# Optimization experiments

Hardware: AMD Instinct MI355X
Metric: run time of the kernel (lower is better)

The kernel has to match this reference:

```python
import jax, jax.numpy as jnp
import numpy as np

B, S, D = 2, 2048, 2048
NH, NKV, HD = 16, 4, 128
EPS = 1e-6


def rmsnorm(x, w, eps=EPS):
    # torch.nn.RMSNorm: x * rsqrt(mean(x^2) + eps) * weight
    ms = jnp.mean(jnp.square(x), axis=-1, keepdims=True)
    return x * jax.lax.rsqrt(ms + eps) * w


def apply_rotary_emb(x, freqs_cis):
    # x: (B, S, H, HD); freqs_cis: (S, HD//2, 2) -> pairwise complex rotation (gpt-fast style)
    xs = x.reshape(*x.shape[:-1], -1, 2)          # (B,S,H,HD//2,2)
    fc = freqs_cis[None, :, None, :, :]           # (1,S,1,HD//2,2)
    xr, xi = xs[..., 0], xs[..., 1]
    fr, fi = fc[..., 0], fc[..., 1]
    out = jnp.stack([xr * fr - xi * fi, xi * fr + xr * fi], axis=-1)
    return out.reshape(x.shape)


def setup_inputs() -> dict:
    key = jax.random.key(0)
    ks = jax.random.split(key, 4)
    x = jax.random.normal(ks[0], (B, S, D), dtype=jnp.float32)
    freqs_cis = jax.random.normal(ks[1], (S, HD // 2, 2), dtype=jnp.float32)
    wqkv = jax.random.normal(ks[2], ((NH + 2 * NKV) * HD, D), dtype=jnp.float32) * (D ** -0.5)
    wo = jax.random.normal(ks[3], (NH * HD, D), dtype=jnp.float32).T * ((NH * HD) ** -0.5)
    wo = jnp.asarray(wo)  # (D, NH*HD) torch layout (out,in)
    q_norm_w = jnp.ones((HD,), dtype=jnp.float32)
    k_norm_w = jnp.ones((HD,), dtype=jnp.float32)
    return {"x": x, "freqs_cis": freqs_cis, "wqkv": wqkv, "wo": wo,
            "q_norm_w": q_norm_w, "k_norm_w": k_norm_w}


def reference(x, freqs_cis, wqkv, wo, q_norm_w, k_norm_w):
    b, s, _ = x.shape
    q_size, kv_size = NH * HD, NKV * HD
    qkv = jnp.einsum('bsd,ed->bse', x, wqkv)  # fused QKV projection
    q, k, v = jnp.split(qkv, [q_size, q_size + kv_size], axis=-1)
    q = q.reshape(b, s, NH, HD)
    k = k.reshape(b, s, NKV, HD)
    v = v.reshape(b, s, NKV, HD)
    q = rmsnorm(q, q_norm_w)
    k = rmsnorm(k, k_norm_w)
    q = apply_rotary_emb(q, freqs_cis)
    k = apply_rotary_emb(k, freqs_cis)
    # GQA: repeat_interleave KV heads to NH
    rep = NH // NKV
    k = jnp.repeat(k, rep, axis=2)  # (b,s,NH,HD)
    v = jnp.repeat(v, rep, axis=2)
    scale = 1.0 / np.sqrt(HD)
    scores = jnp.einsum('bqhd,bkhd->bhqk', q, k) * scale
    causal = jnp.tril(jnp.ones((s, s), dtype=bool))
    scores = jnp.where(causal[None, None], scores, -jnp.inf)
    attn = jax.nn.softmax(scores, axis=-1)
    y = jnp.einsum('bhqk,bkhd->bqhd', attn, v)
    y = y.reshape(b, s, q_size)
    return jnp.einsum('bse,de->bsd', y, wo)
```

## Files before the change

kernel.cpp:

```cpp
#include <hip/hip_runtime.h>
#include <math.h>

constexpr int B_ = 2, S_ = 2048, D_ = 2048, NH_ = 16, NKV_ = 4, HD_ = 128;
constexpr int EQKV_ = (NH_ + 2 * NKV_) * HD_;
constexpr int M_ = B_ * S_;
constexpr float EPS_ = 1e-6f;
constexpr float QSCALE_ = 0.08838834764831845f;

typedef __attribute__((ext_vector_type(8))) short bf16x8;
typedef __attribute__((ext_vector_type(4))) float f32x4;
typedef __attribute__((address_space(1))) unsigned int gu32;
typedef __attribute__((address_space(3))) unsigned int lu32;

__device__ inline ushort f2bf(float f) {
    unsigned u = __float_as_uint(f);
    return (ushort)((u + 0x7FFF + ((u >> 16) & 1)) >> 16);
}

__global__ __launch_bounds__(256) void pack_bf16(
    const float* __restrict__ in, ushort* __restrict__ out, int n4)
{
    int i = blockIdx.x * 256 + threadIdx.x;
    if (i >= n4) return;
    float4 f = ((const float4*)in)[i];
    ushort4 u;
    u.x = f2bf(f.x); u.y = f2bf(f.y); u.z = f2bf(f.z); u.w = f2bf(f.w);
    ((ushort4*)out)[i] = u;
}

__global__ __launch_bounds__(256) void gemm_nt_bf16(
    const ushort* __restrict__ A, const ushort* __restrict__ W,
    float* __restrict__ C, int M, int N, int K)
{
    __shared__ ushort As[128 * 32];
    __shared__ ushort Bs[128 * 32];
    const int t = threadIdx.x;
    const int wave = t >> 6, lane = t & 63;
    const int m0 = blockIdx.y * 128, n0 = blockIdx.x * 128;
    const int wm = (wave >> 1) * 64, wn = (wave & 1) * 64;
    const int lrow = lane & 15, lquad = lane >> 4;

    f32x4 acc[4][4];
#pragma unroll
    for (int i = 0; i < 4; ++i)
#pragma unroll
        for (int j = 0; j < 4; ++j) acc[i][j] = (f32x4){0.f, 0.f, 0.f, 0.f};

    for (int k0 = 0; k0 < K; k0 += 32) {
        __syncthreads();
#pragma unroll
        for (int i = 0; i < 2; ++i) {
            int chunk = t + 256 * i;
            int row = chunk >> 2, seg = chunk & 3;
            int ubase = (wave * 64 + 256 * i) * 8;
            __builtin_amdgcn_global_load_lds(
                (const gu32*)(A + (size_t)(m0 + row) * K + k0 + seg * 8),
                (lu32*)(As + ubase), 16, 0, 0);
            __builtin_amdgcn_global_load_lds(
                (const gu32*)(W + (size_t)(n0 + row) * K + k0 + seg * 8),
                (lu32*)(Bs + ubase), 16, 0, 0);
        }
        __syncthreads();

        bf16x8 af[4], bf[4];
#pragma unroll
        for (int i = 0; i < 4; ++i) {
            af[i] = *(const bf16x8*)(As + (wm + i * 16 + lrow) * 32 + lquad * 8);
            bf[i] = *(const bf16x8*)(Bs + (wn + i * 16 + lrow) * 32 + lquad * 8);
        }
#pragma unroll
        for (int i = 0; i < 4; ++i)
#pragma unroll
            for (int j = 0; j < 4; ++j)
                acc[i][j] = __builtin_amdgcn_mfma_f32_16x16x32_bf16(
                    af[i], bf[j], acc[i][j], 0, 0, 0);
    }
#pragma unroll
    for (int i = 0; i < 4; ++i)
#pragma unroll
        for (int j = 0; j < 4; ++j) {
            float* cp = C + (size_t)(m0 + wm + i * 16 + lquad * 4) * N
                          + n0 + wn + j * 16 + lrow;
#pragma unroll
            for (int r = 0; r < 4; ++r) cp[(size_t)r * N] = acc[i][j][r];
        }
}

__global__ __launch_bounds__(128) void norm_rope(
    const float* __restrict__ qkv, const float* __restrict__ freqs,
    const float* __restrict__ qw, const float* __restrict__ kw,
    ushort* __restrict__ qo, ushort* __restrict__ ko, ushort* __restrict__ vo)
{
    const int bs = blockIdx.x;
    const int head = blockIdx.y;
    const int d = threadIdx.x;
    const int b = bs >> 11, s = bs & (S_ - 1);
    const float x = qkv[(size_t)bs * EQKV_ + head * HD_ + d];

    if (head >= NH_ + NKV_) {
        const int vh = head - (NH_ + NKV_);
        vo[((size_t)(b * NKV_ + vh) * HD_ + d) * S_ + s] = f2bf(x);
        return;
    }
    __shared__ float wsum[2];
    float sq = x * x;
#pragma unroll
    for (int off = 1; off < 64; off <<= 1) sq += __shfl_xor(sq, off);
    if ((threadIdx.x & 63) == 0) wsum[threadIdx.x >> 6] = sq;
    __syncthreads();
    const float rs = rsqrtf((wsum[0] + wsum[1]) * (1.0f / HD_) + EPS_);
    const bool isq = head < NH_;
    const float w = isq ? qw[d] : kw[d];
    const float xn = x * rs * w;
    const float other = __shfl_xor(xn, 1);
    const float fr = freqs[s * HD_ + (d & ~1)];
    const float fi = freqs[s * HD_ + (d & ~1) + 1];
    float out = (d & 1) ? fmaf(xn, fr, other * fi)
                        : fmaf(xn, fr, -other * fi);
    if (isq) {
        out *= QSCALE_;
        qo[((size_t)(b * NH_ + head) * S_ + s) * HD_ + d] = f2bf(out);
    } else {
        const int kh = head - NH_;
        ko[((size_t)(b * NKV_ + kh) * S_ + s) * HD_ + d] = f2bf(out);
    }
}

__global__ __launch_bounds__(256, 3) void flash_attn_mfma(
    const ushort* __restrict__ Q,
    const ushort* __restrict__ K,
    const ushort* __restrict__ V,
    ushort* __restrict__ Y)
{
    __shared__ __align__(16) ushort Ks[4 * 64 * 32];
    __shared__ __align__(16) ushort Vs[2 * 128 * 32];
    __shared__ __align__(16) ushort Ps[4 * 16 * 72];

    const int t = threadIdx.x, w = t >> 6, lane = t & 63;
    const int lx = lane & 15, quad = lane >> 4;
    const int h = blockIdx.y, b = blockIdx.z;
    const int qt = (int)gridDim.x - 1 - (int)blockIdx.x;
    const int q0 = qt * 64;
    const int kvh = h >> 2;
    const int srow = lane >> 2, sseg = lane & 3;
    const int wslot = (sseg ^ ((srow >> 1) & 3)) * 8;
    const int rslot = (quad ^ ((lx >> 1) & 3)) * 8;

    const ushort* qb = Q + ((size_t)(b * NH_ + h) * S_ + q0) * HD_;
    const ushort* ksrc = K + ((size_t)(b * NKV_ + kvh) * S_ + w * 16 + srow) * HD_
                           + sseg * 8;
    const ushort* vb = V + ((size_t)(b * NKV_ + kvh) * HD_) * S_;
    const ushort* vsrc0 = vb + (size_t)(w * 16 + srow) * S_ + sseg * 8;
    const ushort* vsrc1 = vb + (size_t)(64 + w * 16 + srow) * S_ + sseg * 8;
    ushort* kdst = Ks + w * 512 + srow * 32 + wslot;
    ushort* vdst0 = Vs + (w * 16 + srow) * 32 + wslot;
    ushort* vdst1 = Vs + (64 + w * 16 + srow) * 32 + wslot;

    bf16x8 aq[4];
#pragma unroll
    for (int ks = 0; ks < 4; ++ks)
        aq[ks] = *(const bf16x8*)(qb + (size_t)(w * 16 + lx) * HD_ + ks * 32 + quad * 8);

    f32x4 o[8];
#pragma unroll
    for (int j = 0; j < 8; ++j) o[j] = (f32x4){0.f, 0.f, 0.f, 0.f};
    float mrow[4] = {-INFINITY, -INFINITY, -INFINITY, -INFINITY};
    float lp[4] = {0.f, 0.f, 0.f, 0.f};

    uint4 kr0, kr1, kr2, kr3, vr0, vr1, vr2, vr3;

    kr0 = *(const uint4*)(ksrc +  0);
    kr1 = *(const uint4*)(ksrc + 32);
    kr2 = *(const uint4*)(ksrc + 64);
    kr3 = *(const uint4*)(ksrc + 96);
    vr0 = *(const uint4*)(vsrc0 +  0);
    vr1 = *(const uint4*)(vsrc1 +  0);
    vr2 = *(const uint4*)(vsrc0 + 32);
    vr3 = *(const uint4*)(vsrc1 + 32);

    const int ntiles = qt + 1;
    for (int tk = 0; tk < ntiles; ++tk) {
        const int k0 = tk * 64;
        asm volatile("s_barrier" ::: "memory");
        *(uint4*)(kdst +    0) = kr0;
        *(uint4*)(kdst + 2048) = kr1;
        *(uint4*)(kdst + 4096) = kr2;
        *(uint4*)(kdst + 6144) = kr3;
        *(uint4*)(vdst0 +    0) = vr0;
        *(uint4*)(vdst1 +    0) = vr1;
        *(uint4*)(vdst0 + 4096) = vr2;
        *(uint4*)(vdst1 + 4096) = vr3;
        asm volatile("s_waitcnt lgkmcnt(0)" ::: "memory");
        asm volatile("s_barrier" ::: "memory");

        if (tk + 1 < ntiles) {
            const size_t ko8 = (size_t)(k0 + 64);
            kr0 = *(const uint4*)(ksrc + ko8 * HD_ +  0);
            kr1 = *(const uint4*)(ksrc + ko8 * HD_ + 32);
            kr2 = *(const uint4*)(ksrc + ko8 * HD_ + 64);
            kr3 = *(const uint4*)(ksrc + ko8 * HD_ + 96);
            vr0 = *(const uint4*)(vsrc0 + ko8 +  0);
            vr1 = *(const uint4*)(vsrc1 + ko8 +  0);
            vr2 = *(const uint4*)(vsrc0 + ko8 + 32);
            vr3 = *(const uint4*)(vsrc1 + ko8 + 32);
        }

        f32x4 s[4];
#pragma unroll
        for (int j = 0; j < 4; ++j) s[j] = (f32x4){0.f, 0.f, 0.f, 0.f};
        __builtin_amdgcn_s_setprio(1);
#pragma unroll
        for (int ks = 0; ks < 4; ++ks) {
#pragma unroll
            for (int j = 0; j < 4; ++j) {
                bf16x8 bk = *(const bf16x8*)(Ks + ks * 2048 + (j * 16 + lx) * 32 + rslot);
                s[j] = __builtin_amdgcn_mfma_f32_16x16x32_bf16(aq[ks], bk, s[j], 0, 0, 0);
            }
        }
        __builtin_amdgcn_s_setprio(0);

        const int qrow_base = q0 + w * 16 + quad * 4;
        if (tk == ntiles - 1) {
#pragma unroll
            for (int reg = 0; reg < 4; ++reg) {
                const int qrow = qrow_base + reg;
#pragma unroll
                for (int j = 0; j < 4; ++j)
                    if (k0 + lx + 16 * j > qrow) s[j][reg] = -INFINITY;
            }
        }

        float rmx[4];
        bool need = false;
#pragma unroll
        for (int reg = 0; reg < 4; ++reg) {
            rmx[reg] = fmaxf(fmaxf(s[0][reg], s[1][reg]),
                             fmaxf(s[2][reg], s[3][reg]));
            need |= (rmx[reg] > mrow[reg] + 8.0f);
        }
        if (__any(need)) {
#pragma unroll
            for (int reg = 0; reg < 4; ++reg) {
                float rm = rmx[reg];
#pragma unroll
                for (int off = 1; off < 16; off <<= 1)
                    rm = fmaxf(rm, __shfl_xor(rm, off));
                const float mn = fmaxf(mrow[reg], rm);
                const float alpha = __expf(mrow[reg] - mn);
                mrow[reg] = mn;
                lp[reg] *= alpha;
#pragma unroll
                for (int j = 0; j < 8; ++j) o[j][reg] *= alpha;
            }
        }
#pragma unroll
        for (int reg = 0; reg < 4; ++reg) {
#pragma unroll
            for (int j = 0; j < 4; ++j) {
                const float p = __expf(s[j][reg] - mrow[reg]);
                lp[reg] += p;
                Ps[w * 1152 + (quad * 4 + reg) * 72 + lx + 16 * j] = f2bf(p);
            }
        }

        bf16x8 ap[2];
#pragma unroll
        for (int ks2 = 0; ks2 < 2; ++ks2)
            ap[ks2] = *(const bf16x8*)(Ps + w * 1152 + lx * 72 + ks2 * 32 + quad * 8);
        __builtin_amdgcn_s_setprio(1);
#pragma unroll
        for (int jd = 0; jd < 8; ++jd) {
#pragma unroll
            for (int ks2 = 0; ks2 < 2; ++ks2) {
                bf16x8 bv = *(const bf16x8*)(Vs + ks2 * 4096 + (jd * 16 + lx) * 32 + rslot);
                o[jd] = __builtin_amdgcn_mfma_f32_16x16x32_bf16(ap[ks2], bv, o[jd], 0, 0, 0);
            }
        }
        __builtin_amdgcn_s_setprio(0);
    }

#pragma unroll
    for (int reg = 0; reg < 4; ++reg) {
        float l = lp[reg];
#pragma unroll
        for (int off = 1; off < 16; off <<= 1) l += __shfl_xor(l, off);
        const float inv = 1.0f / l;
        const size_t yb = (size_t)(b * S_ + q0 + w * 16 + quad * 4 + reg) * (NH_ * HD_)
                        + h * HD_ + lx;
#pragma unroll
        for (int jd = 0; jd < 8; ++jd)
            Y[yb + jd * 16] = f2bf(o[jd][reg] * inv);
    }
}

extern "C" void kernel_launch(void* const* d_in, const int* in_sizes, int n_in,
                              void* d_out, int out_size, void* d_ws, size_t ws_size,
                              hipStream_t stream)
{
    const float* x     = (const float*)d_in[0];
    const float* freqs = (const float*)d_in[1];
    const float* wqkv  = (const float*)d_in[2];
    const float* wo    = (const float*)d_in[3];
    const float* qw    = (const float*)d_in[4];
    const float* kw    = (const float*)d_in[5];
    float* out = (float*)d_out;

    char* ws = (char*)d_ws;
    float*  qkv    = (float*)ws;
    ushort* wqkvbf = (ushort*)(ws + 50331648);
    ushort* xbf    = (ushort*)(ws + 83886080);
    ushort* qbf    = (ushort*)(ws + 50331648);
    ushort* kbf    = (ushort*)(ws + 67108864);
    ushort* vtb    = (ushort*)(ws + 71303168);
    ushort* wobf   = (ushort*)(ws + 0);
    ushort* ybf    = (ushort*)(ws + 8388608);

    pack_bf16<<<(M_ * D_ / 4 + 255) / 256, 256, 0, stream>>>(x, xbf, M_ * D_ / 4);
    pack_bf16<<<(EQKV_ * D_ / 4 + 255) / 256, 256, 0, stream>>>(wqkv, wqkvbf,
                                                                EQKV_ * D_ / 4);
    gemm_nt_bf16<<<dim3(EQKV_ / 128, M_ / 128), 256, 0, stream>>>(
        xbf, wqkvbf, qkv, M_, EQKV_, D_);
    norm_rope<<<dim3(M_, NH_ + 2 * NKV_), 128, 0, stream>>>(qkv, freqs, qw, kw,
                                                            qbf, kbf, vtb);
    pack_bf16<<<(D_ * NH_ * HD_ / 4 + 255) / 256, 256, 0, stream>>>(
        wo, wobf, D_ * NH_ * HD_ / 4);
    flash_attn_mfma<<<dim3(S_ / 64, NH_, B_), 256, 0, stream>>>(qbf, kbf, vtb, ybf);
    gemm_nt_bf16<<<dim3(D_ / 128, M_ / 128), 256, 0, stream>>>(
        ybf, wobf, out, M_, D_, NH_ * HD_);
}
```

Baseline: 400.2 us.

## Fuse QK RMSNorm, RoPE and bf16 packing into QKV GEMM epilogue

Replaces the fp32 QKV GEMM output plus separate norm_rope kernel with a GEMM whose epilogue computes per-head RMSNorm, rotary embedding and scaling, then writes bf16 Q/K and transposed V through shared memory with coalesced stores. Each 128-column tile is one head, so the row sum-of-squares is reduced across the two column waves via shared memory. This removes the 48MB fp32 qkv write and read-back and one kernel launch. In exchange the epilogue is heavier, with scattered freqs loads and extra shared-memory traffic, and the workspace layout is reorganised.

```diff
diff --git a/kernel.cpp b/kernel.cpp
--- a/kernel.cpp
+++ b/kernel.cpp
@@ -86,43 +86,150 @@
         }
 }
 
-__global__ __launch_bounds__(128) void norm_rope(
-    const float* __restrict__ qkv, const float* __restrict__ freqs,
+__global__ __launch_bounds__(256) void gemm_qkv_fused(
+    const ushort* __restrict__ A,
+    const ushort* __restrict__ W,
+    const float* __restrict__ freqs,
     const float* __restrict__ qw, const float* __restrict__ kw,
-    ushort* __restrict__ qo, ushort* __restrict__ ko, ushort* __restrict__ vo)
+    ushort* __restrict__ qo, ushort* __restrict__ ko, ushort* __restrict__ vo,
+    int K)
 {
-    const int bs = blockIdx.x;
-    const int head = blockIdx.y;
-    const int d = threadIdx.x;
-    const int b = bs >> 11, s = bs & (S_ - 1);
-    const float x = qkv[(size_t)bs * EQKV_ + head * HD_ + d];
-
-    if (head >= NH_ + NKV_) {
+    __shared__ __align__(16) ushort smem[128 * 136];
+    __shared__ float rsbuf[256];
+    ushort* As = smem;
+    ushort* Bs = smem + 4096;
+    ushort* Lt = smem;
+
+    const int t = threadIdx.x;
+    const int wave = t >> 6, lane = t & 63;
+    const int m0 = blockIdx.y * 128, n0 = blockIdx.x * 128;
+    const int wm = (wave >> 1) * 64, wn = (wave & 1) * 64;
+    const int half = wave & 1;
+    const int lrow = lane & 15, lquad = lane >> 4;
+    const int head = n0 >> 7;
+    const int b = m0 >> 11, s0 = m0 & (S_ - 1);
+
+    f32x4 acc[4][4];
+#pragma unroll
+    for (int i = 0; i < 4; ++i)
+#pragma unroll
+        for (int j = 0; j < 4; ++j) acc[i][j] = (f32x4){0.f, 0.f, 0.f, 0.f};
+
+    for (int k0 = 0; k0 < K; k0 += 32) {
+        __syncthreads();
+#pragma unroll
+        for (int i = 0; i < 2; ++i) {
+            int chunk = t + 256 * i;
+            int row = chunk >> 2, seg = chunk & 3;
+            int ubase = (wave * 64 + 256 * i) * 8;
+            __builtin_amdgcn_global_load_lds(
+                (const gu32*)(A + (size_t)(m0 + row) * K + k0 + seg * 8),
+                (lu32*)(As + ubase), 16, 0, 0);
+            __builtin_amdgcn_global_load_lds(
+                (const gu32*)(W + (size_t)(n0 + row) * K + k0 + seg * 8),
+                (lu32*)(Bs + ubase), 16, 0, 0);
+        }
+        __syncthreads();
+
+        bf16x8 af[4], bf[4];
+#pragma unroll
+        for (int i = 0; i < 4; ++i) {
+            af[i] = *(const bf16x8*)(As + (wm + i * 16 + lrow) * 32 + lquad * 8);
+            bf[i] = *(const bf16x8*)(Bs + (wn + i * 16 + lrow) * 32 + lquad * 8);
+        }
+#pragma unroll
+        for (int i = 0; i < 4; ++i)
+#pragma unroll
+            for (int j = 0; j < 4; ++j)
+                acc[i][j] = __builtin_amdgcn_mfma_f32_16x16x32_bf16(
+                    af[i], bf[j], acc[i][j], 0, 0, 0);
+    }
+    __syncthreads();
+
+    float part[4][4];
+    if (head < NH_ + NKV_) {
+#pragma unroll
+        for (int i = 0; i < 4; ++i)
+#pragma unroll
+            for (int r = 0; r < 4; ++r) {
+                float p = acc[i][0][r] * acc[i][0][r]
+                        + acc[i][1][r] * acc[i][1][r]
+                        + acc[i][2][r] * acc[i][2][r]
+                        + acc[i][3][r] * acc[i][3][r];
+#pragma unroll
+                for (int off = 1; off < 16; off <<= 1) p += __shfl_xor(p, off);
+                part[i][r] = p;
+                if (lrow == 0)
+                    rsbuf[half * 128 + wm + i * 16 + lquad * 4 + r] = p;
+            }
+    }
+    __syncthreads();
+
+    if (head < NH_ + NKV_) {
+        const float* nw = (head < NH_) ? qw : kw;
+        float wv[4];
+#pragma unroll
+        for (int j = 0; j < 4; ++j) wv[j] = nw[wn + j * 16 + lrow];
+#pragma unroll
+        for (int i = 0; i < 4; ++i)
+#pragma unroll
+            for (int r = 0; r < 4; ++r) {
+                const int rowid = wm + i * 16 + lquad * 4 + r;
+                const int s = s0 + rowid;
+                const float total = part[i][r] + rsbuf[(half ^ 1) * 128 + rowid];
+                const float rs = rsqrtf(total * (1.0f / HD_) + EPS_);
+#pragma unroll
+                for (int j = 0; j < 4; ++j) {
+                    const int d = wn + j * 16 + lrow;
+                    const float xn = acc[i][j][r] * rs * wv[j];
+                    const float other = __shfl_xor(xn, 1);
+                    const float fr = freqs[s * HD_ + (d & ~1)];
+                    const float fi = freqs[s * HD_ + (d & ~1) + 1];
+                    float out = (d & 1) ? fmaf(xn, fr, other * fi)
+                                        : fmaf(xn, fr, -other * fi);
+                    if (head < NH_) out *= QSCALE_;
+                    Lt[rowid * 136 + d] = f2bf(out);
+                }
+            }
+    } else {
+#pragma unroll
+        for (int i = 0; i < 4; ++i)
+#pragma unroll
+            for (int j = 0; j < 4; ++j)
+#pragma unroll
+                for (int r = 0; r < 4; ++r)
+                    Lt[(wn + j * 16 + lrow) * 136 + wm + i * 16 + lquad * 4 + r]
+                        = f2bf(acc[i][j][r]);
+    }
+    __syncthreads();
+
+    const int g = t >> 4, lx16 = t & 15;
+    if (head < NH_) {
+        ushort* dst0 = qo + ((size_t)(b * NH_ + head) * S_ + s0) * HD_;
+#pragma unroll
+        for (int it = 0; it < 8; ++it) {
+            const int rowid = it * 16 + g;
+            uint4 v = *(const uint4*)(Lt + rowid * 136 + lx16 * 8);
+            *(uint4*)(dst0 + (size_t)rowid * HD_ + lx16 * 8) = v;
+        }
+    } else if (head < NH_ + NKV_) {
+        const int kh = head - NH_;
+        ushort* dst0 = ko + ((size_t)(b * NKV_ + kh) * S_ + s0) * HD_;
+#pragma unroll
+        for (int it = 0; it < 8; ++it) {
+            const int rowid = it * 16 + g;
+            uint4 v = *(const uint4*)(Lt + rowid * 136 + lx16 * 8);
+            *(uint4*)(dst0 + (size_t)rowid * HD_ + lx16 * 8) = v;
+        }
+    } else {
         const int vh = head - (NH_ + NKV_);
-        vo[((size_t)(b * NKV_ + vh) * HD_ + d) * S_ + s] = f2bf(x);
-        return;
-    }
-    __shared__ float wsum[2];
-    float sq = x * x;
-#pragma unroll
-    for (int off = 1; off < 64; off <<= 1) sq += __shfl_xor(sq, off);
-    if ((threadIdx.x & 63) == 0) wsum[threadIdx.x >> 6] = sq;
-    __syncthreads();
-    const float rs = rsqrtf((wsum[0] + wsum[1]) * (1.0f / HD_) + EPS_);
-    const bool isq = head < NH_;
-    const float w = isq ? qw[d] : kw[d];
-    const float xn = x * rs * w;
-    const float other = __shfl_xor(xn, 1);
-    const float fr = freqs[s * HD_ + (d & ~1)];
-    const float fi = freqs[s * HD_ + (d & ~1) + 1];
-    float out = (d & 1) ? fmaf(xn, fr, other * fi)
-                        : fmaf(xn, fr, -other * fi);
-    if (isq) {
-        out *= QSCALE_;
-        qo[((size_t)(b * NH_ + head) * S_ + s) * HD_ + d] = f2bf(out);
-    } else {
-        const int kh = head - NH_;
-        ko[((size_t)(b * NKV_ + kh) * S_ + s) * HD_ + d] = f2bf(out);
+        ushort* dst0 = vo + ((size_t)(b * NKV_ + vh) * HD_) * S_ + s0;
+#pragma unroll
+        for (int it = 0; it < 8; ++it) {
+            const int rowid = it * 16 + g;
+            uint4 v = *(const uint4*)(Lt + rowid * 136 + lx16 * 8);
+            *(uint4*)(dst0 + (size_t)rowid * S_ + lx16 * 8) = v;
+        }
     }
 }
 
@@ -168,7 +275,6 @@
     float lp[4] = {0.f, 0.f, 0.f, 0.f};
 
     uint4 kr0, kr1, kr2, kr3, vr0, vr1, vr2, vr3;
-
     kr0 = *(const uint4*)(ksrc +  0);
     kr1 = *(const uint4*)(ksrc + 32);
     kr2 = *(const uint4*)(ksrc + 64);
@@ -306,22 +412,19 @@
     float* out = (float*)d_out;
 
     char* ws = (char*)d_ws;
-    float*  qkv    = (float*)ws;
+    ushort* qbf    = (ushort*)(ws + 0);
+    ushort* kbf    = (ushort*)(ws + 16777216);
+    ushort* vtb    = (ushort*)(ws + 20971520);
+    ushort* ybf    = (ushort*)(ws + 25165824);
+    ushort* wobf   = (ushort*)(ws + 41943040);
     ushort* wqkvbf = (ushort*)(ws + 50331648);
     ushort* xbf    = (ushort*)(ws + 83886080);
-    ushort* qbf    = (ushort*)(ws + 50331648);
-    ushort* kbf    = (ushort*)(ws + 67108864);
-    ushort* vtb    = (ushort*)(ws + 71303168);
-    ushort* wobf   = (ushort*)(ws + 0);
-    ushort* ybf    = (ushort*)(ws + 8388608);
 
     pack_bf16<<<(M_ * D_ / 4 + 255) / 256, 256, 0, stream>>>(x, xbf, M_ * D_ / 4);
     pack_bf16<<<(EQKV_ * D_ / 4 + 255) / 256, 256, 0, stream>>>(wqkv, wqkvbf,
                                                                 EQKV_ * D_ / 4);
-    gemm_nt_bf16<<<dim3(EQKV_ / 128, M_ / 128), 256, 0, stream>>>(
-        xbf, wqkvbf, qkv, M_, EQKV_, D_);
-    norm_rope<<<dim3(M_, NH_ + 2 * NKV_), 128, 0, stream>>>(qkv, freqs, qw, kw,
-                                                            qbf, kbf, vtb);
+    gemm_qkv_fused<<<dim3(EQKV_ / 128, M_ / 128), 256, 0, stream>>>(
+        xbf, wqkvbf, freqs, qw, kw, qbf, kbf, vtb, D_);
     pack_bf16<<<(D_ * NH_ * HD_ / 4 + 255) / 256, 256, 0, stream>>>(
         wo, wobf, D_ * NH_ * HD_ / 4);
     flash_attn_mfma<<<dim3(S_ / 64, NH_, B_), 256, 0, stream>>>(qbf, kbf, vtb, ybf);
```

Measured after the change: 366.2 us. 8.5% less time.
